# Kernel optimization log

Hardware: AMD Instinct MI355X
Metric: run time of the kernel (lower is better)

The kernel has to match this reference:

```python
import jax, jax.numpy as jnp
import numpy as np


def setup_inputs() -> dict:
    key = jax.random.key(0)
    k0, k1, k2, k3 = jax.random.split(key, 4)
    B, T, C = 4, 2048, 1024
    x = jax.random.normal(k0, (B, T, C), dtype=jnp.float32)
    s = C ** -0.5  # init-scale for weights so activations stay O(1)
    Wq = jax.random.normal(k1, (C, C), dtype=jnp.float32) * s
    Wk = jax.random.normal(k2, (C, C), dtype=jnp.float32) * s
    Wv = jax.random.normal(k3, (C, C), dtype=jnp.float32) * s
    return {"x": x, "Wq": Wq, "Wk": Wk, "Wv": Wv}


def reference(x, Wq, Wk, Wv):
    B, T, C = x.shape
    # torch nn.Linear: y = x @ W.T
    q = jnp.einsum('btc,dc->btd', x, Wq)
    k = jnp.einsum('btc,dc->btd', x, Wk)
    v = jnp.einsum('btc,dc->btd', x, Wv)
    scale = C ** -0.5
    wei = jnp.einsum('btd,bsd->bts', q, k) * scale  # [B, T, T]
    causal = jnp.tril(jnp.ones((T, T), dtype=bool))
    wei = jnp.where(causal, wei, -jnp.inf)
    wei = jax.nn.softmax(wei, axis=-1)
    out = jnp.einsum('bts,bsd->btd', wei, v)
    return out
```

## Files before the change

kernel.cpp:

```cpp
#include <hip/hip_runtime.h>
#include <hip/hip_bf16.h>
#include <math.h>

#define B_ 4
#define T_ 2048
#define C_ 1024
#define M_ (B_*T_)

typedef __attribute__((ext_vector_type(8))) __bf16 bf16x8;
typedef __attribute__((ext_vector_type(4))) float floatx4;

__device__ inline float bf2f(unsigned short u){
    return __uint_as_float(((unsigned)u) << 16);
}
__device__ inline unsigned short f2bf(float f){
    unsigned u = __float_as_uint(f);
    unsigned r = (u + 0x7fffu + ((u >> 16) & 1u)) >> 16;
    return (unsigned short)r;
}

__device__ inline void llds16(const unsigned short* g, unsigned short* lds){
    __builtin_amdgcn_global_load_lds(
        (const __attribute__((address_space(1))) unsigned int*)g,
        (__attribute__((address_space(3))) unsigned int*)(unsigned int)(uintptr_t)lds,
        16, 0, 0);
}

#define NX_ (M_*C_/4)
#define NW_ (C_*C_/4)
__global__ __launch_bounds__(256) void cast_all(
    const float* __restrict__ x, const float* __restrict__ wq,
    const float* __restrict__ wk, const float* __restrict__ wv,
    unsigned short* __restrict__ xb, unsigned short* __restrict__ wb)
{
    int i = blockIdx.x * 256 + threadIdx.x;
    const float* src; unsigned short* dst; int idx;
    if (i < NX_){ src = x; dst = xb; idx = i; }
    else {
        i -= NX_;
        int w = i / NW_; idx = i - w * NW_;
        src = (w == 0) ? wq : ((w == 1) ? wk : wv);
        dst = wb + (size_t)w * C_ * C_;
    }
    float4 v = ((const float4*)src)[idx];
    ((ushort4*)dst)[idx] = make_ushort4(f2bf(v.x), f2bf(v.y), f2bf(v.z), f2bf(v.w));
}

template<bool RS>
__device__ inline void gemm_core(const unsigned short* __restrict__ A,
                                 const unsigned short* __restrict__ Bm,
                                 int lda, int ldb, int m0, int n0, int kTiles,
                                 unsigned short* As, unsigned short* Bs,
                                 floatx4 acc[4][4], float rs[4])
{
    const int tid  = threadIdx.x;
    const int lane = tid & 63;
    const int wave = tid >> 6;
    const int wm = (wave >> 1) * 64;
    const int wn = (wave & 1) * 64;
    const int fr = lane & 15;
    const int fq = lane >> 4;
    const int cxor = fr & 7;
    const int srow = wave * 32 + (lane >> 3);
    const int scol = ((lane & 7) ^ ((lane >> 3) & 7)) * 8;

    const unsigned short* gA = A  + (size_t)(m0 + srow) * lda + scol;
    const unsigned short* gB = Bm + (size_t)(n0 + srow) * ldb + scol;
    unsigned short* ldsA = As + wave * 32 * 64;
    unsigned short* ldsB = Bs + wave * 32 * 64;

    for (int kt = 0; kt < kTiles; kt++){
        const int k0 = kt * 64;
        __syncthreads();
        #pragma unroll
        for (int i = 0; i < 4; i++){
            llds16(gA + (size_t)(i * 8) * lda + k0, ldsA + i * 8 * 64);
            llds16(gB + (size_t)(i * 8) * ldb + k0, ldsB + i * 8 * 64);
        }
        __syncthreads();
        #pragma unroll
        for (int ks = 0; ks < 64; ks += 32){
            const int cpos = (((ks >> 3) + fq) ^ cxor) * 8;
            bf16x8 af[4], bv[4];
            #pragma unroll
            for (int i = 0; i < 4; i++)
                af[i] = *(const bf16x8*)(As + (wm + i*16 + fr) * 64 + cpos);
            #pragma unroll
            for (int j = 0; j < 4; j++)
                bv[j] = *(const bf16x8*)(Bs + (wn + j*16 + fr) * 64 + cpos);
            #pragma unroll
            for (int i = 0; i < 4; i++)
                #pragma unroll
                for (int j = 0; j < 4; j++)
                    acc[i][j] = __builtin_amdgcn_mfma_f32_16x16x32_bf16(af[i], bv[j], acc[i][j], 0, 0, 0);
            if (RS){
                #pragma unroll
                for (int i = 0; i < 4; i++)
                    #pragma unroll
                    for (int e = 0; e < 8; e++)
                        rs[i] += (float)af[i][e];
            }
        }
    }
}

#define ACC_INIT floatx4 acc[4][4]; \
    _Pragma("unroll") for (int i = 0; i < 4; i++) \
        _Pragma("unroll") for (int j = 0; j < 4; j++) acc[i][j] = (floatx4){0.f,0.f,0.f,0.f};

__global__ __launch_bounds__(256, 4) void proj_gemm(
    const unsigned short* __restrict__ xb,
    const unsigned short* __restrict__ Wb,
    unsigned short* __restrict__ Qb, unsigned short* __restrict__ Kb,
    unsigned short* __restrict__ Vt)
{
    __shared__ unsigned short As[128 * 64];
    __shared__ unsigned short Bs[128 * 64];
    const int n0 = blockIdx.x * 128;
    const int m0 = blockIdx.y * 128;
    const int z  = blockIdx.z;
    const unsigned short* W = Wb + (size_t)z * C_ * C_;

    ACC_INIT;
    float rs[4];
    gemm_core<false>(xb, W, C_, C_, m0, n0, C_ / 64, As, Bs, acc, rs);

    const int lane = threadIdx.x & 63, wave = threadIdx.x >> 6;
    const int wm = (wave >> 1) * 64, wn = (wave & 1) * 64;
    const int fr = lane & 15, fq = lane >> 4;

    if (z < 2){
        unsigned short* Y = z ? Kb : Qb;
        #pragma unroll
        for (int i = 0; i < 4; i++)
            #pragma unroll
            for (int j = 0; j < 4; j++)
                #pragma unroll
                for (int r = 0; r < 4; r++){
                    int row = m0 + wm + i*16 + fq*4 + r;
                    int col = n0 + wn + j*16 + fr;
                    Y[(size_t)row * C_ + col] = f2bf(acc[i][j][r]);
                }
    } else {
        #pragma unroll
        for (int i = 0; i < 4; i++)
            #pragma unroll
            for (int j = 0; j < 4; j++){
                int row = m0 + wm + i*16 + fq*4;
                int col = n0 + wn + j*16 + fr;
                int b = row / T_, t = row % T_;
                ushort4 o = make_ushort4(f2bf(acc[i][j][0]), f2bf(acc[i][j][1]),
                                         f2bf(acc[i][j][2]), f2bf(acc[i][j][3]));
                *(ushort4*)&Vt[(size_t)b * C_ * T_ + (size_t)col * T_ + t] = o;
            }
    }
}

__global__ __launch_bounds__(256, 4) void score_gemm(
    const unsigned short* __restrict__ Qb, const unsigned short* __restrict__ Kb,
    unsigned short* __restrict__ P)
{
    int idx = blockIdx.x;
    int ti = (int)((sqrtf(8.f * idx + 1.f) - 1.f) * 0.5f);
    while ((ti + 1) * (ti + 2) / 2 <= idx) ti++;
    while (ti * (ti + 1) / 2 > idx) ti--;
    const int si = idx - ti * (ti + 1) / 2;
    const int t0 = ti * 128, s0 = si * 128;
    const int b  = blockIdx.y;

    __shared__ unsigned short As[128 * 64];
    __shared__ unsigned short Bs[128 * 64];
    ACC_INIT;
    float rs[4];
    gemm_core<false>(Qb + (size_t)b * T_ * C_, Kb + (size_t)b * T_ * C_,
                     C_, C_, t0, s0, C_ / 64, As, Bs, acc, rs);

    const int lane = threadIdx.x & 63, wave = threadIdx.x >> 6;
    const int wm = (wave >> 1) * 64, wn = (wave & 1) * 64;
    const int fr = lane & 15, fq = lane >> 4;
    unsigned short* Pb = P + (size_t)b * T_ * T_;
    const float scale = 0.03125f;
    #pragma unroll
    for (int i = 0; i < 4; i++)
        #pragma unroll
        for (int j = 0; j < 4; j++)
            #pragma unroll
            for (int r = 0; r < 4; r++){
                int t = t0 + wm + i*16 + fq*4 + r;
                int s = s0 + wn + j*16 + fr;
                float v = (s <= t) ? __expf(acc[i][j][r] * scale) : 0.f;
                Pb[(size_t)t * T_ + s] = f2bf(v);
            }
}

__global__ __launch_bounds__(256, 4) void pv_gemm(
    const unsigned short* __restrict__ P, const unsigned short* __restrict__ Vt,
    float* __restrict__ out)
{
    const int n0 = blockIdx.x * 128;
    const int t0 = (gridDim.y - 1 - blockIdx.y) * 128;
    const int b  = blockIdx.z;
    __shared__ unsigned short As[128 * 64];
    __shared__ unsigned short Bs[128 * 64];
    __shared__ float lsum[128];

    ACC_INIT;
    float rs[4] = {0.f, 0.f, 0.f, 0.f};
    const int kTiles = (t0 + 128) / 64;
    gemm_core<true>(P + (size_t)b * T_ * T_, Vt + (size_t)b * C_ * T_,
                    T_, T_, t0, n0, kTiles, As, Bs, acc, rs);

    const int lane = threadIdx.x & 63, wave = threadIdx.x >> 6;
    const int wm = (wave >> 1) * 64, wn = (wave & 1) * 64;
    const int fr = lane & 15, fq = lane >> 4;

    #pragma unroll
    for (int i = 0; i < 4; i++){
        float v = rs[i];
        v += __shfl_xor(v, 16, 64);
        v += __shfl_xor(v, 32, 64);
        rs[i] = v;
    }
    if (fq == 0){
        #pragma unroll
        for (int i = 0; i < 4; i++) lsum[wm + i*16 + fr] = rs[i];
    }
    __syncthreads();

    float* ob = out + (size_t)b * T_ * C_;
    #pragma unroll
    for (int i = 0; i < 4; i++){
        float inv[4];
        #pragma unroll
        for (int r = 0; r < 4; r++) inv[r] = 1.f / lsum[wm + i*16 + fq*4 + r];
        #pragma unroll
        for (int j = 0; j < 4; j++)
            #pragma unroll
            for (int r = 0; r < 4; r++){
                int t = t0 + wm + i*16 + fq*4 + r;
                int d = n0 + wn + j*16 + fr;
                ob[(size_t)t * C_ + d] = acc[i][j][r] * inv[r];
            }
    }
}

extern "C" void kernel_launch(void* const* d_in, const int* in_sizes, int n_in,
                              void* d_out, int out_size, void* d_ws, size_t ws_size,
                              hipStream_t stream)
{
    const float* x  = (const float*)d_in[0];
    const float* Wq = (const float*)d_in[1];
    const float* Wk = (const float*)d_in[2];
    const float* Wv = (const float*)d_in[3];
    float* out = (float*)d_out;

    unsigned short* Qb = (unsigned short*)d_ws;
    unsigned short* Kb = Qb + (size_t)M_ * C_;
    unsigned short* Vt = Kb + (size_t)M_ * C_;
    unsigned short* P  = Vt + (size_t)M_ * C_;
    unsigned short* xb = P;
    unsigned short* Wb = P + (size_t)M_ * C_;

    cast_all<<<(NX_ + 3 * NW_ + 255) / 256, 256, 0, stream>>>(x, Wq, Wk, Wv, xb, Wb);
    proj_gemm <<<dim3(8, 64, 3), 256, 0, stream>>>(xb, Wb, Qb, Kb, Vt);
    score_gemm<<<dim3(136, 4),   256, 0, stream>>>(Qb, Kb, P);
    pv_gemm   <<<dim3(8, 16, 4), 256, 0, stream>>>(P, Vt, out);
}
```

Measured before the change: 242.4 us.

## Remap block indices to balance causal work and improve XCD cache locality

All three GEMM kernels move to 1D grids, and the block index is decoded so that consecutive blocks (L&7) spread across the 8 XCDs. Blocks that land on the same XCD share m-tiles or work on nearby tiles, which should improve L2 reuse. For the causal score and PV kernels, each XCD is given a paired set of long and short rows (ti = 15-k and ti = k) so every XCD gets a similar amount of work. This depends on the hardware's round-robin dispatch of blocks to XCDs, and it also changes the order in which blocks are scheduled.

New measurement: 218.1 us. -10.0%, faster.

```diff
diff --git a/kernel.cpp b/kernel.cpp
--- a/kernel.cpp
+++ b/kernel.cpp
@@ -116,9 +116,11 @@
 {
     __shared__ unsigned short As[128 * 64];
     __shared__ unsigned short Bs[128 * 64];
-    const int n0 = blockIdx.x * 128;
-    const int m0 = blockIdx.y * 128;
-    const int z  = blockIdx.z;
+    const int L = blockIdx.x;
+    const int k = L & 7, j = L >> 3;
+    const int m0 = (k * 8 + (j & 7)) * 128;
+    const int n0 = ((j >> 3) & 7) * 128;
+    const int z  = j >> 6;
     const unsigned short* W = Wb + (size_t)z * C_ * C_;
 
     ACC_INIT;
@@ -134,23 +136,23 @@
         #pragma unroll
         for (int i = 0; i < 4; i++)
             #pragma unroll
-            for (int j = 0; j < 4; j++)
+            for (int jj = 0; jj < 4; jj++)
                 #pragma unroll
                 for (int r = 0; r < 4; r++){
                     int row = m0 + wm + i*16 + fq*4 + r;
-                    int col = n0 + wn + j*16 + fr;
-                    Y[(size_t)row * C_ + col] = f2bf(acc[i][j][r]);
+                    int col = n0 + wn + jj*16 + fr;
+                    Y[(size_t)row * C_ + col] = f2bf(acc[i][jj][r]);
                 }
     } else {
         #pragma unroll
         for (int i = 0; i < 4; i++)
             #pragma unroll
-            for (int j = 0; j < 4; j++){
+            for (int jj = 0; jj < 4; jj++){
                 int row = m0 + wm + i*16 + fq*4;
-                int col = n0 + wn + j*16 + fr;
+                int col = n0 + wn + jj*16 + fr;
                 int b = row / T_, t = row % T_;
-                ushort4 o = make_ushort4(f2bf(acc[i][j][0]), f2bf(acc[i][j][1]),
-                                         f2bf(acc[i][j][2]), f2bf(acc[i][j][3]));
+                ushort4 o = make_ushort4(f2bf(acc[i][jj][0]), f2bf(acc[i][jj][1]),
+                                         f2bf(acc[i][jj][2]), f2bf(acc[i][jj][3]));
                 *(ushort4*)&Vt[(size_t)b * C_ * T_ + (size_t)col * T_ + t] = o;
             }
     }
@@ -160,13 +162,13 @@
     const unsigned short* __restrict__ Qb, const unsigned short* __restrict__ Kb,
     unsigned short* __restrict__ P)
 {
-    int idx = blockIdx.x;
-    int ti = (int)((sqrtf(8.f * idx + 1.f) - 1.f) * 0.5f);
-    while ((ti + 1) * (ti + 2) / 2 <= idx) ti++;
-    while (ti * (ti + 1) / 2 > idx) ti--;
-    const int si = idx - ti * (ti + 1) / 2;
+    const int L = blockIdx.x;
+    const int k = L & 7, j = L >> 3;
+    const int b = j / 17, r = j % 17;
+    int ti, si;
+    if (r <= 15 - k){ ti = 15 - k; si = r; }
+    else            { ti = k;      si = r - (16 - k); }
     const int t0 = ti * 128, s0 = si * 128;
-    const int b  = blockIdx.y;
 
     __shared__ unsigned short As[128 * 64];
     __shared__ unsigned short Bs[128 * 64];
@@ -183,12 +185,12 @@
     #pragma unroll
     for (int i = 0; i < 4; i++)
         #pragma unroll
-        for (int j = 0; j < 4; j++)
-            #pragma unroll
-            for (int r = 0; r < 4; r++){
-                int t = t0 + wm + i*16 + fq*4 + r;
-                int s = s0 + wn + j*16 + fr;
-                float v = (s <= t) ? __expf(acc[i][j][r] * scale) : 0.f;
+        for (int jj = 0; jj < 4; jj++)
+            #pragma unroll
+            for (int r2 = 0; r2 < 4; r2++){
+                int t = t0 + wm + i*16 + fq*4 + r2;
+                int s = s0 + wn + jj*16 + fr;
+                float v = (s <= t) ? __expf(acc[i][jj][r2] * scale) : 0.f;
                 Pb[(size_t)t * T_ + s] = f2bf(v);
             }
 }
@@ -197,9 +199,13 @@
     const unsigned short* __restrict__ P, const unsigned short* __restrict__ Vt,
     float* __restrict__ out)
 {
-    const int n0 = blockIdx.x * 128;
-    const int t0 = (gridDim.y - 1 - blockIdx.y) * 128;
-    const int b  = blockIdx.z;
+    const int L = blockIdx.x;
+    const int k = L & 7, j = L >> 3;
+    const int b = j >> 4, r = j & 15;
+    const int n0 = (r >> 1) * 128;
+    const int ti = (r & 1) ? k : (15 - k);
+    const int t0 = ti * 128;
+
     __shared__ unsigned short As[128 * 64];
     __shared__ unsigned short Bs[128 * 64];
     __shared__ float lsum[128];
@@ -232,14 +238,14 @@
     for (int i = 0; i < 4; i++){
         float inv[4];
         #pragma unroll
-        for (int r = 0; r < 4; r++) inv[r] = 1.f / lsum[wm + i*16 + fq*4 + r];
-        #pragma unroll
-        for (int j = 0; j < 4; j++)
-            #pragma unroll
-            for (int r = 0; r < 4; r++){
-                int t = t0 + wm + i*16 + fq*4 + r;
-                int d = n0 + wn + j*16 + fr;
-                ob[(size_t)t * C_ + d] = acc[i][j][r] * inv[r];
+        for (int r2 = 0; r2 < 4; r2++) inv[r2] = 1.f / lsum[wm + i*16 + fq*4 + r2];
+        #pragma unroll
+        for (int jj = 0; jj < 4; jj++)
+            #pragma unroll
+            for (int r2 = 0; r2 < 4; r2++){
+                int t = t0 + wm + i*16 + fq*4 + r2;
+                int d = n0 + wn + jj*16 + fr;
+                ob[(size_t)t * C_ + d] = acc[i][jj][r2] * inv[r2];
             }
     }
 }
@@ -262,7 +268,7 @@
     unsigned short* Wb = P + (size_t)M_ * C_;
 
     cast_all<<<(NX_ + 3 * NW_ + 255) / 256, 256, 0, stream>>>(x, Wq, Wk, Wv, xb, Wb);
-    proj_gemm <<<dim3(8, 64, 3), 256, 0, stream>>>(xb, Wb, Qb, Kb, Vt);
-    score_gemm<<<dim3(136, 4),   256, 0, stream>>>(Qb, Kb, P);
-    pv_gemm   <<<dim3(8, 16, 4), 256, 0, stream>>>(P, Vt, out);
-}
+    proj_gemm <<<1536, 256, 0, stream>>>(xb, Wb, Qb, Kb, Vt);
+    score_gemm<<<544,  256, 0, stream>>>(Qb, Kb, P);
+    pv_gemm   <<<512,  256, 0, stream>>>(P, Vt, out);
+}
```
